# Kernel tuning notes

Hardware: AMD Instinct MI355X
Metric: run time of the kernel (lower is better)

## Reference

```python
import jax, jax.numpy as jnp
import numpy as np

D_MODEL = 256
D_STATE = 16
D_CONV = 3
D_INNER = 256          # expand=1
D_HALF = D_INNER // 2  # 128
DT_RANK = 16           # ceil(256/16)
B, L0, L1 = 4, 4096, 4096


def setup_inputs() -> dict:
    key = jax.random.key(0)
    ks = jax.random.split(key, 10)
    u_0 = jax.random.normal(ks[0], (B, L0, D_MODEL), jnp.float32)
    u_1 = jax.random.normal(ks[1], (B, L1, D_MODEL), jnp.float32)
    in_proj_w = jax.random.normal(ks[2], (D_INNER, D_MODEL), jnp.float32) * (D_MODEL ** -0.5)
    conv_x_w = jax.random.normal(ks[3], (D_HALF, 1, D_CONV), jnp.float32) * (D_CONV ** -0.5)
    conv_z_w = jax.random.normal(ks[4], (D_HALF, 1, D_CONV), jnp.float32) * (D_CONV ** -0.5)
    x_proj_w = jax.random.normal(ks[5], (DT_RANK + 2 * D_STATE, D_HALF), jnp.float32) * (D_HALF ** -0.5)
    dt_init_std = DT_RANK ** -0.5
    dt_proj_w = jax.random.uniform(ks[6], (D_HALF, DT_RANK), jnp.float32, -dt_init_std, dt_init_std)
    # dt bias = inverse-softplus of dt ~ LogUniform(1e-3, 1e-1)
    dt = jnp.exp(jax.random.uniform(ks[7], (D_HALF,), jnp.float32) * (np.log(0.1) - np.log(0.001)) + np.log(0.001))
    dt = jnp.clip(dt, 1e-4, None)
    dt_proj_b = dt + jnp.log(-jnp.expm1(-dt))
    A_log = jnp.log(jnp.broadcast_to(jnp.arange(1, D_STATE + 1, dtype=jnp.float32), (D_HALF, D_STATE)))
    D_param = jnp.ones((D_HALF,), jnp.float32)
    out_proj_w = jax.random.normal(ks[8], (D_MODEL, D_INNER), jnp.float32) * (D_INNER ** -0.5)
    return {"u_0": u_0, "u_1": u_1, "in_proj_w": in_proj_w, "conv_x_w": conv_x_w,
            "conv_z_w": conv_z_w, "x_proj_w": x_proj_w, "dt_proj_w": dt_proj_w,
            "dt_proj_b": dt_proj_b, "A_log": A_log, "D": D_param, "out_proj_w": out_proj_w}


def _dwconv(x, w):
    # x: [B, C, L], w: [C, 1, K] depthwise, padding='same', no bias (conv_bias//2 == 0)
    return jax.lax.conv_general_dilated(
        x, w, window_strides=(1,), padding='SAME',
        feature_group_count=x.shape[1], dimension_numbers=('NCH', 'OIH', 'NCH'))


def _selective_scan(u, delta, A, Bm, Cm, Dv):
    # u, delta: [B, L, d]; A: [d, n]; Bm, Cm: [B, L, n]; Dv: [d]
    dA = jnp.exp(delta[..., None] * A)                       # [B, L, d, n]
    dBu = (delta * u)[..., None] * Bm[:, :, None, :]         # [B, L, d, n]
    def combine(c1, c2):
        a1, b1 = c1
        a2, b2 = c2
        return a2 * a1, a2 * b1 + b2
    _, h = jax.lax.associative_scan(combine, (dA, dBu), axis=1)  # h: [B, L, d, n]
    return jnp.einsum('bldn,bln->bld', h, Cm) + u * Dv


def _stream(u, in_proj_w, conv_x_w, conv_z_w, x_proj_w, dt_proj_w, dt_proj_b, A, D, out_proj_w):
    xz = jnp.einsum('bld,ed->ble', u, in_proj_w)             # [B, L, d_inner]
    x, z = jnp.split(xz, 2, axis=-1)                         # [B, L, d_half] each
    x = jnp.swapaxes(x, 1, 2)                                # [B, d_half, L]
    z = jnp.swapaxes(z, 1, 2)
    x_f = jax.nn.silu(_dwconv(x, conv_x_w))
    z_f = jax.nn.silu(_dwconv(z, conv_z_w))
    xf = jnp.swapaxes(x_f, 1, 2)                             # [B, L, d_half]
    dbl = jnp.einsum('bld,ed->ble', xf, x_proj_w)            # [B, L, dt_rank + 2n]
    dt, Bm, Cm = jnp.split(dbl, [DT_RANK, DT_RANK + D_STATE], axis=-1)
    dt = jnp.einsum('blr,dr->bld', dt, dt_proj_w)
    delta = jax.nn.softplus(dt + dt_proj_b)                  # delta_bias + delta_softplus
    y = _selective_scan(xf, delta, A, Bm, Cm, D)             # [B, L, d_half]
    cat = jnp.concatenate([y, jnp.swapaxes(z_f, 1, 2)], axis=-1)  # [B, L, d_inner]
    return jnp.einsum('ble,oe->blo', cat, out_proj_w)


def reference(u_0, u_1, in_proj_w, conv_x_w, conv_z_w, x_proj_w, dt_proj_w, dt_proj_b, A_log, D, out_proj_w):
    A = -jnp.exp(A_log)
    out0 = _stream(u_0, in_proj_w, conv_x_w, conv_z_w, x_proj_w, dt_proj_w, dt_proj_b, A, D, out_proj_w)
    out1 = _stream(u_1, in_proj_w, conv_x_w, conv_z_w, x_proj_w, dt_proj_w, dt_proj_b, A, D, out_proj_w)
    return (out0, out1)
```

## Files before the change

### kernel.cpp

```cpp
#include <hip/hip_runtime.h>
#include <hip/hip_bf16.h>
#include <cstdint>

#define DEV __device__ __forceinline__

typedef __attribute__((ext_vector_type(8))) short short8;
typedef __attribute__((ext_vector_type(4))) float f32x4;
typedef __attribute__((ext_vector_type(4))) unsigned short us4;
typedef __attribute__((ext_vector_type(8))) unsigned short us8;

DEV unsigned short f2bf(float x) {
    unsigned int u = __float_as_uint(x);
    unsigned int r = (u + 0x7FFFu + ((u >> 16) & 1u)) >> 16;
    return (unsigned short)r;
}
DEV float bf2f(unsigned short h) { return __uint_as_float(((unsigned int)h) << 16); }

DEV void gld_lds16(const unsigned short* g, unsigned short* l) {
    __builtin_amdgcn_global_load_lds(
        (const __attribute__((address_space(1))) unsigned int*)g,
        (__attribute__((address_space(3))) unsigned int*)l, 16, 0, 0);
}

DEV float silu(float v) {
    return __fdividef(v, 1.f + __expf(-v));
}

DEV float fexp2(float x) {
    float r;
    asm("v_exp_f32 %0, %1" : "=v"(r) : "v"(x));
    return r;
}

DEV void lds_barrier() {
    __builtin_amdgcn_sched_barrier(0);
    asm volatile("s_waitcnt lgkmcnt(0)" ::: "memory");
    __builtin_amdgcn_s_barrier();
    __builtin_amdgcn_sched_barrier(0);
}

#define LL 4096
#define DM 256
#define DH 128
#define SB_TOT 8
#define CH1 32
#define NCH 128
#define LOG2E 1.44269504088896f

__global__ __launch_bounds__(256) void prep_kernel(
    const float* __restrict__ u0, const float* __restrict__ u1,
    const float* __restrict__ inw, const float* __restrict__ outw,
    const float* __restrict__ xpw, const float* __restrict__ dtw,
    unsigned short* __restrict__ ubf, unsigned short* __restrict__ wbi,
    unsigned short* __restrict__ wbo, unsigned short* __restrict__ Wb)
{
    int gid = blockIdx.x * 256 + threadIdx.x;
    int i = gid * 4;
    if (i < 4194304) {
        f32x4 v = *(const f32x4*)&u0[i];
        us4 r = { f2bf(v.x), f2bf(v.y), f2bf(v.z), f2bf(v.w) };
        *(us4*)&ubf[i] = r;
    } else if (i < 8388608) {
        int j = i - 4194304;
        f32x4 v = *(const f32x4*)&u1[j];
        us4 r = { f2bf(v.x), f2bf(v.y), f2bf(v.z), f2bf(v.w) };
        *(us4*)&ubf[4194304 + j] = r;
    } else if (i < 8454144) {
        int j = i - 8388608;
        f32x4 v = *(const f32x4*)&inw[j];
        us4 r = { f2bf(v.x), f2bf(v.y), f2bf(v.z), f2bf(v.w) };
        *(us4*)&wbi[j] = r;
    } else if (i < 8519680) {
        int j = i - 8454144;
        f32x4 v = *(const f32x4*)&outw[j];
        us4 r = { f2bf(v.x), f2bf(v.y), f2bf(v.z), f2bf(v.w) };
        *(us4*)&wbo[j] = r;
    } else if (i < 8540160) {
        int j = i - 8519680;
        int n = j >> 7, k0 = j & 127;
        if (n < 128) {
            float a0 = 0.f, a1 = 0.f, a2 = 0.f, a3 = 0.f;
            const float* dw = dtw + n * 16;
            #pragma unroll
            for (int r = 0; r < 16; ++r) {
                float w = dw[r];
                const float* xr = xpw + r * 128 + k0;
                a0 = fmaf(w, xr[0], a0);
                a1 = fmaf(w, xr[1], a1);
                a2 = fmaf(w, xr[2], a2);
                a3 = fmaf(w, xr[3], a3);
            }
            us4 rr = { f2bf(a0), f2bf(a1), f2bf(a2), f2bf(a3) };
            *(us4*)&Wb[n * 128 + k0] = rr;
        } else {
            f32x4 v = *(const f32x4*)&xpw[(n - 112) * 128 + k0];
            us4 rr = { f2bf(v.x), f2bf(v.y), f2bf(v.z), f2bf(v.w) };
            *(us4*)&Wb[n * 128 + k0] = rr;
        }
    }
}

template<int F32OUT>
__global__ __launch_bounds__(256) void gemm_bt(
    const unsigned short* __restrict__ A, const unsigned short* __restrict__ B,
    float* __restrict__ Cf, unsigned short* __restrict__ Cb)
{
    __shared__ __align__(16) unsigned short As[128 * 32];
    __shared__ __align__(16) unsigned short Bs[128 * 32];
    const int t = threadIdx.x;
    const int m0 = blockIdx.x * 128, n0 = blockIdx.y * 128;
    const int lane = t & 63, wv = t >> 6;
    const int wm = (wv & 1) * 64, wn = (wv >> 1) * 64;
    const int lr = lane & 15, lk = (lane >> 4) * 8;
    const int srow = lane >> 2, scol = (lane & 3) * 8;

    f32x4 acc[4][4] = {};
    for (int kt = 0; kt < 8; ++kt) {
        const int k0 = kt * 32;
        #pragma unroll
        for (int h = 0; h < 2; ++h) {
            const int c = wv + h * 4;
            const unsigned short* ga = A + (size_t)(m0 + c * 16 + srow) * 256 + k0 + scol;
            const unsigned short* gb = B + (size_t)(n0 + c * 16 + srow) * 256 + k0 + scol;
            gld_lds16(ga, &As[c * 512]);
            gld_lds16(gb, &Bs[c * 512]);
        }
        __syncthreads();
        short8 av[4], bv[4];
        #pragma unroll
        for (int i = 0; i < 4; ++i) av[i] = *(const short8*)&As[(wm + i * 16 + lr) * 32 + lk];
        #pragma unroll
        for (int i = 0; i < 4; ++i) bv[i] = *(const short8*)&Bs[(wn + i * 16 + lr) * 32 + lk];
        #pragma unroll
        for (int i = 0; i < 4; ++i)
            #pragma unroll
            for (int j = 0; j < 4; ++j)
                acc[i][j] = __builtin_amdgcn_mfma_f32_16x16x32_bf16(av[i], bv[j], acc[i][j], 0, 0, 0);
        __syncthreads();
    }
    #pragma unroll
    for (int i = 0; i < 4; ++i) {
        #pragma unroll
        for (int j = 0; j < 4; ++j) {
            int r0 = m0 + wm + i * 16 + (lane >> 4) * 4;
            int cc = n0 + wn + j * 16 + lr;
            #pragma unroll
            for (int r = 0; r < 4; ++r) {
                float v = acc[i][j][r];
                if (F32OUT) Cf[(size_t)(r0 + r) * 256 + cc] = v;
                else        Cb[(size_t)(r0 + r) * 256 + cc] = f2bf(v);
            }
        }
    }
}

template<int FUSE_SCAN>
__global__ __launch_bounds__(256) void convproj_k(
    const unsigned short* __restrict__ xz, const unsigned short* __restrict__ Wb,
    const float* __restrict__ wx, const float* __restrict__ wz,
    const float* __restrict__ dtb, const float* __restrict__ alog,
    float* __restrict__ xf, unsigned short* __restrict__ catb,
    float* __restrict__ delta, float* __restrict__ BC,
    float* __restrict__ P, float* __restrict__ H)
{
    __shared__ __align__(16) char smem[35840];
    unsigned short* As = (unsigned short*)smem;
    float* dl_s = (float*)smem;
    float* xf_s = (float*)(smem + 16896);
    float* bc_s = (float*)(smem + 33792);
    const int t = threadIdx.x;
    const int kk = blockIdx.x & 7, yy = blockIdx.x >> 3;
    const int m0 = (4 * kk + (yy & 3) + 32 * (yy >> 2)) * 32;

    const int gg = t & 31;
    const bool isx = gg < 16;
    const int c = (isx ? gg : gg - 16) * 8;
    const float* wp = isx ? wx : wz;
    float wreg[24];
    #pragma unroll
    for (int j = 0; j < 6; ++j) *(f32x4*)&wreg[j * 4] = *(const f32x4*)(wp + c * 3 + j * 4);
    #pragma unroll
    for (int i = 0; i < 4; ++i) {
        int r = (t >> 5) + i * 8;
        int gr = m0 + r;
        int l = gr & 4095;
        const unsigned short* bp = xz + (size_t)gr * 256 + (isx ? c : 128 + c);
        us8 zz = (us8)0;
        us8 vm = (l > 0)    ? *(const us8*)(bp - 256) : zz;
        us8 v0 = *(const us8*)bp;
        us8 vp = (l < 4095) ? *(const us8*)(bp + 256) : zz;
        float o[8];
        #pragma unroll
        for (int j = 0; j < 8; ++j) {
            float v = bf2f(vm[j]) * wreg[j * 3] + bf2f(v0[j]) * wreg[j * 3 + 1]
                    + bf2f(vp[j]) * wreg[j * 3 + 2];
            o[j] = silu(v);
        }
        us8 rb8 = { f2bf(o[0]), f2bf(o[1]), f2bf(o[2]), f2bf(o[3]),
                    f2bf(o[4]), f2bf(o[5]), f2bf(o[6]), f2bf(o[7]) };
        if (isx) {
            *(us8*)&As[r * 136 + c] = rb8;
            *(f32x4*)&xf_s[r * 132 + c]     = *(f32x4*)&o[0];
            *(f32x4*)&xf_s[r * 132 + c + 4] = *(f32x4*)&o[4];
            *(f32x4*)&xf[(size_t)gr * 128 + c]     = *(f32x4*)&o[0];
            *(f32x4*)&xf[(size_t)gr * 128 + c + 4] = *(f32x4*)&o[4];
        } else {
            *(us8*)&catb[(size_t)gr * 256 + 128 + c] = rb8;
        }
    }
    lds_barrier();
    const int lane = t & 63, wv = t >> 6;
    const int lr = lane & 15, lk = (lane >> 4) * 8;
    const int rt = (wv & 1) * 16;
    const int jbase = (wv >> 1) * 5;
    f32x4 acc[5] = {};
    #pragma unroll
    for (int kt = 0; kt < 4; ++kt) {
        const int k0 = kt * 32;
        short8 av = *(const short8*)&As[(rt + lr) * 136 + k0 + lk];
        #pragma unroll
        for (int j = 0; j < 5; ++j) {
            short8 bv = *(const short8*)(Wb + ((jbase + j) * 16 + lr) * 128 + k0 + lk);
            acc[j] = __builtin_amdgcn_mfma_f32_16x16x32_bf16(av, bv, acc[j], 0, 0, 0);
        }
    }
    lds_barrier();
    const int r0 = (lane >> 4) * 4;
    #pragma unroll
    for (int j = 0; j < 5; ++j) {
        int jj = jbase + j;
        int col = jj * 16 + lr;
        #pragma unroll
        for (int r = 0; r < 4; ++r) {
            float v = acc[j][r];
            int lrow = rt + r0 + r;
            size_t row = (size_t)m0 + lrow;
            if (jj < 8) {
                float x = v + dtb[col];
                float sp = (x > 20.f) ? x : __logf(1.f + __expf(x));
                delta[row * 128 + col] = sp;
                if (FUSE_SCAN) dl_s[lrow * 132 + col] = sp;
            } else {
                BC[row * 32 + (col - 128)] = v;
                if (FUSE_SCAN && jj == 8) bc_s[lrow * 16 + lr] = v;
            }
        }
    }
    if (!FUSE_SCAN) return;

    lds_barrier();
    const int hh = t >> 7, tl = t & 127;
    const int sb = m0 >> 12;
    const int ch = (m0 & 4095) >> 5;
    float Ar[8];
    #pragma unroll
    for (int n = 0; n < 8; ++n) Ar[n] = -__expf(alog[tl * 16 + hh * 8 + n]) * LOG2E;
    float h[8], p[8];
    #pragma unroll
    for (int n = 0; n < 8; ++n) { h[n] = 0.f; p[n] = 1.f; }
    #pragma unroll 4
    for (int i = 0; i < CH1; ++i) {
        float dt = dl_s[i * 132 + tl];
        float du = dt * xf_s[i * 132 + tl];
        float bl[8];
        *(f32x4*)&bl[0] = *(const f32x4*)&bc_s[i * 16 + hh * 8];
        *(f32x4*)&bl[4] = *(const f32x4*)&bc_s[i * 16 + hh * 8 + 4];
        #pragma unroll
        for (int n = 0; n < 8; ++n) {
            float a = fexp2(dt * Ar[n]);
            h[n] = fmaf(a, h[n], du * bl[n]);
            p[n] *= a;
        }
    }
    size_t ob = (((size_t)sb * NCH + ch) * 128 + tl) * 16 + hh * 8;
    f32x4 pv0 = { p[0], p[1], p[2], p[3] };
    f32x4 pv1 = { p[4], p[5], p[6], p[7] };
    f32x4 hv0 = { h[0], h[1], h[2], h[3] };
    f32x4 hv1 = { h[4], h[5], h[6], h[7] };
    *(f32x4*)&P[ob]     = pv0;
    *(f32x4*)&P[ob + 4] = pv1;
    *(f32x4*)&H[ob]     = hv0;
    *(f32x4*)&H[ob + 4] = hv1;
}

__global__ __launch_bounds__(128) void scan_p1(
    const float* __restrict__ delta, const float* __restrict__ xf,
    const float* __restrict__ BC, const float* __restrict__ alog,
    float* __restrict__ P, float* __restrict__ H)
{
    __shared__ float b_s[CH1 * 16];
    int t = threadIdx.x;
    int ch = blockIdx.x, sb = blockIdx.y;
    size_t rb = (size_t)sb * LL + (size_t)ch * CH1;
    {
        int row = t >> 2, c4 = (t & 3) * 4;
        *(f32x4*)&b_s[row * 16 + c4] = *(const f32x4*)&BC[(rb + row) * 32 + c4];
    }
    lds_barrier();
    float Ar[16];
    #pragma unroll
    for (int n = 0; n < 16; ++n) Ar[n] = -__expf(alog[t * 16 + n]) * LOG2E;
    float dtr[32], ur[32];
    #pragma unroll
    for (int i = 0; i < 32; ++i) dtr[i] = delta[(rb + i) * DH + t];
    #pragma unroll
    for (int i = 0; i < 32; ++i) ur[i] = xf[(rb + i) * DH + t];
    float h[16], p[16];
    #pragma unroll
    for (int n = 0; n < 16; ++n) { h[n] = 0.f; p[n] = 1.f; }
    for (int i = 0; i < CH1; ++i) {
        float dt = dtr[i];
        float du = dt * ur[i];
        float bl[16];
        *(f32x4*)&bl[0]  = *(const f32x4*)&b_s[i * 16];
        *(f32x4*)&bl[4]  = *(const f32x4*)&b_s[i * 16 + 4];
        *(f32x4*)&bl[8]  = *(const f32x4*)&b_s[i * 16 + 8];
        *(f32x4*)&bl[12] = *(const f32x4*)&b_s[i * 16 + 12];
        #pragma unroll
        for (int n = 0; n < 16; ++n) {
            float a = fexp2(dt * Ar[n]);
            h[n] = fmaf(a, h[n], du * bl[n]);
            p[n] *= a;
        }
    }
    size_t ob = (((size_t)sb * NCH + ch) * 128 + t) * 16;
    #pragma unroll
    for (int n4 = 0; n4 < 16; n4 += 4) {
        f32x4 pv = { p[n4], p[n4 + 1], p[n4 + 2], p[n4 + 3] };
        f32x4 hv = { h[n4], h[n4 + 1], h[n4 + 2], h[n4 + 3] };
        *(f32x4*)&P[ob + n4] = pv;
        *(f32x4*)&H[ob + n4] = hv;
    }
}

__global__ __launch_bounds__(256) void scan_p2(const float* __restrict__ P, float* __restrict__ H)
{
    __shared__ float Ps[NCH * 16], Hs[NCH * 16];
    int t = threadIdx.x;
    int d = blockIdx.x, sb = blockIdx.y;
    for (int q = t; q < NCH * 4; q += 256) {
        int ch = q >> 2, c4 = (q & 3) * 4;
        size_t g = (((size_t)sb * NCH + ch) * 128 + d) * 16 + c4;
        *(f32x4*)&Ps[ch * 16 + c4] = *(const f32x4*)&P[g];
        *(f32x4*)&Hs[ch * 16 + c4] = *(const f32x4*)&H[g];
    }
    lds_barrier();
    if (t < 16) {
        float hin = 0.f;
        for (int c = 0; c < NCH; ++c) {
            float pp = Ps[c * 16 + t], hl = Hs[c * 16 + t];
            Hs[c * 16 + t] = hin;
            hin = fmaf(pp, hin, hl);
        }
    }
    lds_barrier();
    for (int q = t; q < NCH * 4; q += 256) {
        int ch = q >> 2, c4 = (q & 3) * 4;
        size_t g = (((size_t)sb * NCH + ch) * 128 + d) * 16 + c4;
        *(f32x4*)&H[g] = *(const f32x4*)&Hs[ch * 16 + c4];
    }
}

__global__ __launch_bounds__(128) void scan_p3(
    const float* __restrict__ delta, const float* __restrict__ xf,
    const float* __restrict__ BC, const float* __restrict__ alog,
    const float* __restrict__ Dp, const float* __restrict__ H,
    unsigned short* __restrict__ catb)
{
    __shared__ float b_s[CH1 * 16];
    __shared__ float c_s[CH1 * 16];
    int t = threadIdx.x;
    int ch = blockIdx.x, sb = blockIdx.y;
    size_t rb = (size_t)sb * LL + (size_t)ch * CH1;
    {
        int row = t >> 2, c4 = (t & 3) * 4;
        *(f32x4*)&b_s[row * 16 + c4] = *(const f32x4*)&BC[(rb + row) * 32 + c4];
        *(f32x4*)&c_s[row * 16 + c4] = *(const f32x4*)&BC[(rb + row) * 32 + 16 + c4];
    }
    lds_barrier();
    float Ar[16];
    #pragma unroll
    for (int n = 0; n < 16; ++n) Ar[n] = -__expf(alog[t * 16 + n]) * LOG2E;
    float Dv = Dp[t];
    float dtr[32], ur[32];
    #pragma unroll
    for (int i = 0; i < 32; ++i) dtr[i] = delta[(rb + i) * DH + t];
    #pragma unroll
    for (int i = 0; i < 32; ++i) ur[i] = xf[(rb + i) * DH + t];
    size_t ob = (((size_t)sb * NCH + ch) * 128 + t) * 16;
    float h[16];
    #pragma unroll
    for (int n4 = 0; n4 < 16; n4 += 4) {
        f32x4 hv = *(const f32x4*)&H[ob + n4];
        h[n4] = hv.x; h[n4 + 1] = hv.y; h[n4 + 2] = hv.z; h[n4 + 3] = hv.w;
    }
    for (int i = 0; i < CH1; ++i) {
        float dt = dtr[i];
        float uu = ur[i];
        float du = dt * uu;
        float bl[16], cl[16];
        *(f32x4*)&bl[0]  = *(const f32x4*)&b_s[i * 16];
        *(f32x4*)&bl[4]  = *(const f32x4*)&b_s[i * 16 + 4];
        *(f32x4*)&bl[8]  = *(const f32x4*)&b_s[i * 16 + 8];
        *(f32x4*)&bl[12] = *(const f32x4*)&b_s[i * 16 + 12];
        *(f32x4*)&cl[0]  = *(const f32x4*)&c_s[i * 16];
        *(f32x4*)&cl[4]  = *(const f32x4*)&c_s[i * 16 + 4];
        *(f32x4*)&cl[8]  = *(const f32x4*)&c_s[i * 16 + 8];
        *(f32x4*)&cl[12] = *(const f32x4*)&c_s[i * 16 + 12];
        float y0 = uu * Dv, y1 = 0.f, y2 = 0.f, y3 = 0.f;
        #pragma unroll
        for (int n = 0; n < 16; n += 4) {
            float a0 = fexp2(dt * Ar[n]);
            float a1 = fexp2(dt * Ar[n + 1]);
            float a2 = fexp2(dt * Ar[n + 2]);
            float a3 = fexp2(dt * Ar[n + 3]);
            h[n]     = fmaf(a0, h[n],     du * bl[n]);
            h[n + 1] = fmaf(a1, h[n + 1], du * bl[n + 1]);
            h[n + 2] = fmaf(a2, h[n + 2], du * bl[n + 2]);
            h[n + 3] = fmaf(a3, h[n + 3], du * bl[n + 3]);
            y0 = fmaf(h[n],     cl[n],     y0);
            y1 = fmaf(h[n + 1], cl[n + 1], y1);
            y2 = fmaf(h[n + 2], cl[n + 2], y2);
            y3 = fmaf(h[n + 3], cl[n + 3], y3);
        }
        float y = (y0 + y1) + (y2 + y3);
        catb[(rb + i) * DM + t] = f2bf(y);
    }
}

extern "C" void kernel_launch(void* const* d_in, const int* in_sizes, int n_in,
                              void* d_out, int out_size, void* d_ws, size_t ws_size,
                              hipStream_t stream) {
    const float* u0   = (const float*)d_in[0];
    const float* u1   = (const float*)d_in[1];
    const float* inw  = (const float*)d_in[2];
    const float* cxw  = (const float*)d_in[3];
    const float* czw  = (const float*)d_in[4];
    const float* xpw  = (const float*)d_in[5];
    const float* dtw  = (const float*)d_in[6];
    const float* dtb  = (const float*)d_in[7];
    const float* alog = (const float*)d_in[8];
    const float* Dp   = (const float*)d_in[9];
    const float* outw = (const float*)d_in[10];

    char* ws = (char*)d_ws;
    unsigned short* ubf  = (unsigned short*)(ws + 0);
    float* delta         = (float*)(ws + 0);
    unsigned short* xzbf = (unsigned short*)(ws + 16777216);
    float* P_a           = (float*)(ws + 16777216);
    float* H_a           = (float*)(ws + 25165824);
    float* xf            = (float*)(ws + 33554432);
    float* BC            = (float*)(ws + 50331648);
    unsigned short* catb = (unsigned short*)(ws + 54525952);
    unsigned short* wbi  = (unsigned short*)(ws + 71303168);
    unsigned short* wbo  = (unsigned short*)(ws + 71434240);
    unsigned short* Wb   = (unsigned short*)(ws + 71565312);
    float* P_f           = (float*)(ws + 71606272);
    float* H_f           = (float*)(ws + 79994880);

    float* outp = (float*)d_out;

    prep_kernel<<<8340, 256, 0, stream>>>(u0, u1, inw, outw, xpw, dtw, ubf, wbi, wbo, Wb);
    gemm_bt<0><<<dim3(256, 2), 256, 0, stream>>>(ubf, wbi, nullptr, xzbf);

    if (ws_size >= 88383488ull) {
        convproj_k<1><<<1024, 256, 0, stream>>>(xzbf, Wb, cxw, czw, dtb, alog,
                                                xf, catb, delta, BC, P_f, H_f);
        scan_p2<<<dim3(128, 8), 256, 0, stream>>>(P_f, H_f);
        scan_p3<<<dim3(NCH, 8), 128, 0, stream>>>(delta, xf, BC, alog, Dp, H_f, catb);
    } else {
        convproj_k<0><<<1024, 256, 0, stream>>>(xzbf, Wb, cxw, czw, dtb, alog,
                                                xf, catb, delta, BC, nullptr, nullptr);
        scan_p1<<<dim3(NCH, 8), 128, 0, stream>>>(delta, xf, BC, alog, P_a, H_a);
        scan_p2<<<dim3(128, 8), 256, 0, stream>>>(P_a, H_a);
        scan_p3<<<dim3(NCH, 8), 128, 0, stream>>>(delta, xf, BC, alog, Dp, H_a, catb);
    }
    gemm_bt<1><<<dim3(256, 2), 256, 0, stream>>>(catb, wbo, outp, nullptr);
}
```

Measured before the change: 194.0 us.

## Fuse scan phase 3 with output projection GEMM via MFMA in LDS

The final scan pass now writes y into a shared-memory tile along with the z half of catb, then runs the out_proj matmul directly with bf16 MFMA per 32-row chunk and writes the fp32 output. This removes the separate output GEMM launch and the catb y-half round trip through global memory. In exchange, each 128-thread block re-reads the full out_proj weight from global/L2 without LDS staging, and occupancy may drop from the larger LDS footprint and 16 accumulator vectors.

After: 208.6 us. 7.5% more time.

```diff
diff --git a/kernel.cpp b/kernel.cpp
--- a/kernel.cpp
+++ b/kernel.cpp
@@ -361,14 +361,16 @@
     }
 }
 
-__global__ __launch_bounds__(128) void scan_p3(
+__global__ __launch_bounds__(128) void scan_out(
     const float* __restrict__ delta, const float* __restrict__ xf,
+    const unsigned short* __restrict__ catb,
     const float* __restrict__ BC, const float* __restrict__ alog,
     const float* __restrict__ Dp, const float* __restrict__ H,
-    unsigned short* __restrict__ catb)
+    const unsigned short* __restrict__ wbo, float* __restrict__ outp)
 {
     __shared__ float b_s[CH1 * 16];
     __shared__ float c_s[CH1 * 16];
+    __shared__ __align__(16) unsigned short cat_s[32 * 264];
     int t = threadIdx.x;
     int ch = blockIdx.x, sb = blockIdx.y;
     size_t rb = (size_t)sb * LL + (size_t)ch * CH1;
@@ -376,6 +378,11 @@
         int row = t >> 2, c4 = (t & 3) * 4;
         *(f32x4*)&b_s[row * 16 + c4] = *(const f32x4*)&BC[(rb + row) * 32 + c4];
         *(f32x4*)&c_s[row * 16 + c4] = *(const f32x4*)&BC[(rb + row) * 32 + 16 + c4];
+    }
+    for (int q = t; q < 512; q += 128) {
+        int row = q >> 4, c8 = (q & 15) * 8;
+        *(us8*)&cat_s[row * 264 + 128 + c8] =
+            *(const us8*)&catb[(rb + row) * 256 + 128 + c8];
     }
     lds_barrier();
     float Ar[16];
@@ -424,6 +431,96 @@
             y3 = fmaf(h[n + 3], cl[n + 3], y3);
         }
         float y = (y0 + y1) + (y2 + y3);
+        cat_s[i * 264 + t] = f2bf(y);
+    }
+    lds_barrier();
+    const int lane = t & 63, wv = t >> 6;
+    const int lr = lane & 15, lk = (lane >> 4) * 8;
+    const int rt = wv * 16;
+    f32x4 acc[16] = {};
+    for (int kt = 0; kt < 8; ++kt) {
+        const int k0 = kt * 32;
+        short8 av = *(const short8*)&cat_s[(rt + lr) * 264 + k0 + lk];
+        #pragma unroll
+        for (int j = 0; j < 16; ++j) {
+            short8 bv = *(const short8*)(wbo + (size_t)(j * 16 + lr) * 256 + k0 + lk);
+            acc[j] = __builtin_amdgcn_mfma_f32_16x16x32_bf16(av, bv, acc[j], 0, 0, 0);
+        }
+    }
+    const int r0 = (lane >> 4) * 4;
+    #pragma unroll
+    for (int j = 0; j < 16; ++j) {
+        int cc = j * 16 + lr;
+        #pragma unroll
+        for (int r = 0; r < 4; ++r) {
+            outp[(rb + rt + r0 + r) * 256 + cc] = acc[j][r];
+        }
+    }
+}
+
+__global__ __launch_bounds__(128) void scan_p3(
+    const float* __restrict__ delta, const float* __restrict__ xf,
+    const float* __restrict__ BC, const float* __restrict__ alog,
+    const float* __restrict__ Dp, const float* __restrict__ H,
+    unsigned short* __restrict__ catb)
+{
+    __shared__ float b_s[CH1 * 16];
+    __shared__ float c_s[CH1 * 16];
+    int t = threadIdx.x;
+    int ch = blockIdx.x, sb = blockIdx.y;
+    size_t rb = (size_t)sb * LL + (size_t)ch * CH1;
+    {
+        int row = t >> 2, c4 = (t & 3) * 4;
+        *(f32x4*)&b_s[row * 16 + c4] = *(const f32x4*)&BC[(rb + row) * 32 + c4];
+        *(f32x4*)&c_s[row * 16 + c4] = *(const f32x4*)&BC[(rb + row) * 32 + 16 + c4];
+    }
+    lds_barrier();
+    float Ar[16];
+    #pragma unroll
+    for (int n = 0; n < 16; ++n) Ar[n] = -__expf(alog[t * 16 + n]) * LOG2E;
+    float Dv = Dp[t];
+    float dtr[32], ur[32];
+    #pragma unroll
+    for (int i = 0; i < 32; ++i) dtr[i] = delta[(rb + i) * DH + t];
+    #pragma unroll
+    for (int i = 0; i < 32; ++i) ur[i] = xf[(rb + i) * DH + t];
+    size_t ob = (((size_t)sb * NCH + ch) * 128 + t) * 16;
+    float h[16];
+    #pragma unroll
+    for (int n4 = 0; n4 < 16; n4 += 4) {
+        f32x4 hv = *(const f32x4*)&H[ob + n4];
+        h[n4] = hv.x; h[n4 + 1] = hv.y; h[n4 + 2] = hv.z; h[n4 + 3] = hv.w;
+    }
+    for (int i = 0; i < CH1; ++i) {
+        float dt = dtr[i];
+        float uu = ur[i];
+        float du = dt * uu;
+        float bl[16], cl[16];
+        *(f32x4*)&bl[0]  = *(const f32x4*)&b_s[i * 16];
+        *(f32x4*)&bl[4]  = *(const f32x4*)&b_s[i * 16 + 4];
+        *(f32x4*)&bl[8]  = *(const f32x4*)&b_s[i * 16 + 8];
+        *(f32x4*)&bl[12] = *(const f32x4*)&b_s[i * 16 + 12];
+        *(f32x4*)&cl[0]  = *(const f32x4*)&c_s[i * 16];
+        *(f32x4*)&cl[4]  = *(const f32x4*)&c_s[i * 16 + 4];
+        *(f32x4*)&cl[8]  = *(const f32x4*)&c_s[i * 16 + 8];
+        *(f32x4*)&cl[12] = *(const f32x4*)&c_s[i * 16 + 12];
+        float y0 = uu * Dv, y1 = 0.f, y2 = 0.f, y3 = 0.f;
+        #pragma unroll
+        for (int n = 0; n < 16; n += 4) {
+            float a0 = fexp2(dt * Ar[n]);
+            float a1 = fexp2(dt * Ar[n + 1]);
+            float a2 = fexp2(dt * Ar[n + 2]);
+            float a3 = fexp2(dt * Ar[n + 3]);
+            h[n]     = fmaf(a0, h[n],     du * bl[n]);
+            h[n + 1] = fmaf(a1, h[n + 1], du * bl[n + 1]);
+            h[n + 2] = fmaf(a2, h[n + 2], du * bl[n + 2]);
+            h[n + 3] = fmaf(a3, h[n + 3], du * bl[n + 3]);
+            y0 = fmaf(h[n],     cl[n],     y0);
+            y1 = fmaf(h[n + 1], cl[n + 1], y1);
+            y2 = fmaf(h[n + 2], cl[n + 2], y2);
+            y3 = fmaf(h[n + 3], cl[n + 3], y3);
+        }
+        float y = (y0 + y1) + (y2 + y3);
         catb[(rb + i) * DM + t] = f2bf(y);
     }
 }
@@ -467,13 +564,14 @@
         convproj_k<1><<<1024, 256, 0, stream>>>(xzbf, Wb, cxw, czw, dtb, alog,
                                                 xf, catb, delta, BC, P_f, H_f);
         scan_p2<<<dim3(128, 8), 256, 0, stream>>>(P_f, H_f);
-        scan_p3<<<dim3(NCH, 8), 128, 0, stream>>>(delta, xf, BC, alog, Dp, H_f, catb);
+        scan_out<<<dim3(NCH, 8), 128, 0, stream>>>(delta, xf, catb, BC, alog,
+                                                   Dp, H_f, wbo, outp);
     } else {
         convproj_k<0><<<1024, 256, 0, stream>>>(xzbf, Wb, cxw, czw, dtb, alog,
                                                 xf, catb, delta, BC, nullptr, nullptr);
         scan_p1<<<dim3(NCH, 8), 128, 0, stream>>>(delta, xf, BC, alog, P_a, H_a);
         scan_p2<<<dim3(128, 8), 256, 0, stream>>>(P_a, H_a);
         scan_p3<<<dim3(NCH, 8), 128, 0, stream>>>(delta, xf, BC, alog, Dp, H_a, catb);
-    }
-    gemm_bt<1><<<dim3(256, 2), 256, 0, stream>>>(catb, wbo, outp, nullptr);
-}
+        gemm_bt<1><<<dim3(256, 2), 256, 0, stream>>>(catb, wbo, outp, nullptr);
+    }
+}
```
